# Kernel tuning notes

Hardware: AMD Instinct MI355X
Metric: run time of the kernel (lower is better)

The kernel has to match this reference:

```python
import jax, jax.numpy as jnp
import numpy as np

NUM_CLASSES = 21
THRESH = 0.5
NEG_POS = 3
VAR0, VAR1 = 0.1, 0.2  # SSD cfg['variance']
B, P, O = 32, 32768, 50


def point_form(boxes):
    # center form (cx,cy,w,h) -> corner form (xmin,ymin,xmax,ymax)
    return jnp.concatenate([boxes[:, :2] - boxes[:, 2:] / 2,
                            boxes[:, :2] + boxes[:, 2:] / 2], axis=1)


def jaccard(box_a, box_b):
    # box_a [A,4], box_b [B,4], corner form -> IoU [A,B]
    max_xy = jnp.minimum(box_a[:, None, 2:], box_b[None, :, 2:])
    min_xy = jnp.maximum(box_a[:, None, :2], box_b[None, :, :2])
    inter = jnp.prod(jnp.clip(max_xy - min_xy, 0.0, None), axis=2)
    area_a = jnp.prod(box_a[:, 2:] - box_a[:, :2], axis=1)[:, None]
    area_b = jnp.prod(box_b[:, 2:] - box_b[:, :2], axis=1)[None, :]
    return inter / (area_a + area_b - inter)


def encode(matched, priors):
    # matched corner form [P,4], priors center form [P,4]
    g_cxcy = ((matched[:, :2] + matched[:, 2:]) / 2 - priors[:, :2]) / (VAR0 * priors[:, 2:])
    g_wh = jnp.log((matched[:, 2:] - matched[:, :2]) / priors[:, 2:]) / VAR1
    return jnp.concatenate([g_cxcy, g_wh], axis=1)


def match_one(truths, labels, priors):
    # truths [O,4] corner, labels [O], priors [P,4] center
    overlaps = jaccard(truths, point_form(priors))          # [O,P]
    best_prior_idx = jnp.argmax(overlaps, axis=1)           # [O]
    best_truth_overlap = jnp.max(overlaps, axis=0)          # [P]
    best_truth_idx = jnp.argmax(overlaps, axis=0)           # [P]
    # ensure every gt matches its best prior
    best_truth_overlap = best_truth_overlap.at[best_prior_idx].set(2.0)
    best_truth_idx = best_truth_idx.at[best_prior_idx].set(jnp.arange(truths.shape[0]))
    matches = truths[best_truth_idx]                        # [P,4]
    conf = (labels[best_truth_idx] + 1.0).astype(jnp.int32)
    conf = jnp.where(best_truth_overlap < THRESH, 0, conf)
    return encode(matches, priors), conf


def setup_inputs() -> dict:
    key = jax.random.key(0)
    k1, k2, k3, k4, k5, k6 = jax.random.split(key, 6)
    loc_data = jax.random.normal(k1, (B, P, 4), dtype=jnp.float32)
    conf_data = jax.random.normal(k2, (B, P, NUM_CLASSES), dtype=jnp.float32)
    # priors in center form: centers in (0,1), sizes in (0.02, 0.5)
    cxy = jax.random.uniform(k3, (P, 2), dtype=jnp.float32)
    wh = jax.random.uniform(k4, (P, 2), dtype=jnp.float32, minval=0.02, maxval=0.5)
    priors = jnp.concatenate([cxy, wh], axis=1)
    # targets: valid corner-form boxes + label
    pts = jax.random.uniform(k5, (B, O, 2, 2), dtype=jnp.float32)
    xymin = pts.min(axis=2)
    xymax = jnp.maximum(pts.max(axis=2), xymin + 0.01)
    labels = jax.random.randint(k6, (B, O), 0, NUM_CLASSES - 1).astype(jnp.float32)
    targets = jnp.concatenate([xymin, xymax, labels[..., None]], axis=-1)
    return {"loc_data": loc_data, "conf_data": conf_data, "priors": priors, "targets": targets}


def reference(loc_data, conf_data, priors, targets):
    truths = targets[..., :4]
    labels = targets[..., 4]
    loc_t, conf_t = jax.vmap(match_one, in_axes=(0, 0, None))(truths, labels, priors)
    loc_t = jax.lax.stop_gradient(loc_t)
    conf_t = jax.lax.stop_gradient(conf_t)

    pos = conf_t > 0                                         # [B,P]
    # localization: smooth-L1, summed over positives
    diff = loc_data - loc_t
    ad = jnp.abs(diff)
    sl1 = jnp.where(ad < 1.0, 0.5 * diff * diff, ad - 0.5)
    loss_l = jnp.sum(sl1 * pos[..., None].astype(sl1.dtype))

    # per-prior softmax CE (logsumexp - true logit)
    lse = jax.nn.logsumexp(conf_data, axis=-1)               # [B,P]
    true_logit = jnp.take_along_axis(conf_data, conf_t[..., None], axis=-1)[..., 0]
    ce = lse - true_logit                                    # [B,P]

    # hard negative mining: rank negatives by CE (pos zeroed out)
    ce_mine = jnp.where(pos, 0.0, ce)
    loss_idx = jnp.argsort(-ce_mine, axis=1)
    idx_rank = jnp.argsort(loss_idx, axis=1)
    num_pos = jnp.sum(pos, axis=1, keepdims=True)            # [B,1]
    num_neg = jnp.clip(NEG_POS * num_pos, None, pos.shape[1] - 1)
    neg = idx_rank < num_neg

    sel = pos | neg
    loss_c = jnp.sum(jnp.where(sel, ce, 0.0))

    N = jnp.sum(num_pos).astype(loss_l.dtype)
    return loss_l / N, loss_c / N
```

## Files before the change

### kernel.cpp

```cpp
#include <hip/hip_runtime.h>
#include <math.h>

#define BB 32
#define PP 32768
#define OO 50
#define NC 21
#define MPT 4

#define WBINLO (104 << 7)
#define WBINS  2048

typedef unsigned long long u64;
typedef unsigned int u32;
typedef unsigned char u8;

static constexpr size_t OFF_WHC   = 0;
static constexpr size_t OFF_WHS   = OFF_WHC  + 4ull*BB*WBINS;
static constexpr size_t OFF_KEYS  = OFF_WHS  + 4ull*BB*WBINS;
static constexpr size_t OFF_NPOS  = OFF_KEYS + 8ull*BB*OO;
static constexpr size_t OFF_DACC  = OFF_NPOS + 128;
static constexpr size_t ZERO_BYTES = OFF_DACC + 8ull*3*BB;
static constexpr size_t OFF_BTOV  = (ZERO_BYTES + 127) & ~127ull;
static constexpr size_t OFF_BTIDX = OFF_BTOV  + 4ull*BB*PP;

static __device__ __forceinline__ float fast_div(float a, float b) {
    return a * __builtin_amdgcn_rcpf(b);
}

__global__ __launch_bounds__(256) void match_kernel(
    const float* __restrict__ priors, const float* __restrict__ targets,
    float* __restrict__ btov, u8* __restrict__ btidx, u64* __restrict__ keys)
{
#pragma clang fp contract(off)
    const int b = blockIdx.y;
    const int tid = threadIdx.x;
    const int lane = tid & 63, wid = tid >> 6;
    const int wbase = blockIdx.x * (256 * MPT) + wid * (64 * MPT);

    __shared__ float tr[OO * 5];
    __shared__ u64 wkeys[4][OO];
    if (tid < OO * 5) tr[tid] = targets[(size_t)b * OO * 5 + tid];
    __syncthreads();

    float px1[MPT], py1[MPT], px2[MPT], py2[MPT], area_p[MPT];
#pragma unroll
    for (int s = 0; s < MPT; ++s) {
        int p = wbase + s * 64 + lane;
        float4 pr = *(const float4*)(priors + (size_t)p * 4);
        px1[s] = pr.x - pr.z * 0.5f; py1[s] = pr.y - pr.w * 0.5f;
        px2[s] = pr.x + pr.z * 0.5f; py2[s] = pr.y + pr.w * 0.5f;
        area_p[s] = (px2[s] - px1[s]) * (py2[s] - py1[s]);
    }

    float bestv[MPT]; int besto[MPT];
#pragma unroll
    for (int s = 0; s < MPT; ++s) { bestv[s] = -1.0f; besto[s] = 0; }

    for (int o = 0; o < OO; ++o) {
        float tx1 = tr[o*5+0], ty1 = tr[o*5+1], tx2 = tr[o*5+2], ty2 = tr[o*5+3];
        float area_t = (tx2 - tx1) * (ty2 - ty1);
        float iou[MPT];
#pragma unroll
        for (int s = 0; s < MPT; ++s) {
            float ix1 = fmaxf(tx1, px1[s]), iy1 = fmaxf(ty1, py1[s]);
            float ix2 = fminf(tx2, px2[s]), iy2 = fminf(ty2, py2[s]);
            float dx = fmaxf(ix2 - ix1, 0.0f), dy = fmaxf(iy2 - iy1, 0.0f);
            float inter = dx * dy;
            iou[s] = fast_div(inter, (area_t + area_p[s]) - inter);
            if (iou[s] > bestv[s]) { bestv[s] = iou[s]; besto[s] = o; }
        }
        float mv = fmaxf(fmaxf(iou[0], iou[1]), fmaxf(iou[2], iou[3]));
        for (int m = 1; m < 64; m <<= 1)
            mv = fmaxf(mv, __shfl_xor(mv, m, 64));
        u64 b0 = __ballot(iou[0] == mv);
        u64 b1 = __ballot(iou[1] == mv);
        u64 b2 = __ballot(iou[2] == mv);
        u64 b3 = __ballot(iou[3] == mv);
        if (lane == 0) {
            int s, l;
            if      (b0) { s = 0; l = __ffsll(b0) - 1; }
            else if (b1) { s = 1; l = __ffsll(b1) - 1; }
            else if (b2) { s = 2; l = __ffsll(b2) - 1; }
            else if (b3) { s = 3; l = __ffsll(b3) - 1; }
            else         { s = 0; l = 0; }
            u32 wp = (u32)(wbase + s * 64 + l);
            wkeys[wid][o] = ((u64)__float_as_uint(mv) << 32) | (u64)(0xFFFFFFFFu - wp);
        }
    }
#pragma unroll
    for (int s = 0; s < MPT; ++s) {
        int p = wbase + s * 64 + lane;
        btov[(size_t)b * PP + p] = bestv[s];
        btidx[(size_t)b * PP + p] = (u8)besto[s];
    }
    __syncthreads();
    if (tid < OO) {
        u64 k0 = wkeys[0][tid];
        for (int w = 1; w < 4; ++w) { u64 kw = wkeys[w][tid]; if (kw > k0) k0 = kw; }
        atomicMax(&keys[b * OO + tid], k0);
    }
}

__global__ void override_kernel(const u64* __restrict__ keys,
                                float* __restrict__ btov, u8* __restrict__ btidx) {
    const int b = blockIdx.x;
    const int o = threadIdx.x;
    u32 p = 0xFFFFFFFFu;
    if (o < OO) p = 0xFFFFFFFFu - (u32)(keys[b * OO + o] & 0xFFFFFFFFull);
    bool win = (o < OO);
    for (int o2 = 1; o2 < OO; ++o2) {
        u32 p2 = __shfl(p, o2, 64);
        if (o < o2 && p2 == p) win = false;
    }
    if (win) {
        btov[(size_t)b * PP + p] = 2.0f;
        btidx[(size_t)b * PP + p] = (u8)o;
    }
}

static __device__ __forceinline__ u32 top16bits(float v) {
    u32 u = __float_as_uint(v);
    return (v > 0.0f) ? u : 0u;
}

#define EL(k) ((((k) & 3) == 0) ? v[(k) >> 2].x : \
               (((k) & 3) == 1) ? v[(k) >> 2].y : \
               (((k) & 3) == 2) ? v[(k) >> 2].z : v[(k) >> 2].w)

__global__ __launch_bounds__(256) void score_kernel(
    const float* __restrict__ loc, const float* __restrict__ conf,
    const float* __restrict__ priors, const float* __restrict__ targets,
    const float* __restrict__ btov, const u8* __restrict__ btidx,
    int* __restrict__ npos, double* __restrict__ dacc,
    u32* __restrict__ whc, float* __restrict__ whs)
{
    const int b = blockIdx.y;
    const int tid = threadIdx.x;
    const int p = blockIdx.x * 1024 + tid * 4;
    __shared__ float tr[OO * 5];
    __shared__ __align__(16) u32 hh[WBINS];
    __shared__ __align__(16) float hs[WBINS];
    if (tid < OO * 5) tr[tid] = targets[(size_t)b * OO * 5 + tid];
#pragma unroll
    for (int j = 0; j < WBINS / 256; ++j) { hh[j * 256 + tid] = 0; hs[j * 256 + tid] = 0.0f; }
    __syncthreads();

    float4 ov4 = *(const float4*)(btov + (size_t)b * PP + p);
    uchar4 ox4 = *(const uchar4*)(btidx + (size_t)b * PP + p);
    const float ovv[4] = {ov4.x, ov4.y, ov4.z, ov4.w};
    const int  oidx[4] = {(int)ox4.x, (int)ox4.y, (int)ox4.z, (int)ox4.w};

    const float4* cp = (const float4*)(conf + ((size_t)b * PP + p) * NC);
    float4 v[21];
    float cev[4];
    double l_l = 0.0, pce = 0.0; int np_ = 0;

#pragma unroll
    for (int r = 0; r < 4; ++r) {
        const int jlo = (r == 0) ? 0 : ((21 * (r - 1) + 20) / 4 + 1);
        const int jhi = (21 * r + 20) / 4;
#pragma unroll
        for (int j = jlo; j <= jhi; ++j) v[j] = cp[j];

        int conft = 0;
        if (ovv[r] >= 0.5f) conft = (int)(tr[oidx[r] * 5 + 4] + 1.0f);
        const bool pos = conft > 0;

        float m = -1e30f;
#pragma unroll
        for (int c = 0; c < NC; ++c) m = fmaxf(m, EL(21 * r + c));
        float s = 0.0f, tl = 0.0f;
#pragma unroll
        for (int c = 0; c < NC; ++c) {
            float xx = EL(21 * r + c);
            s += expf(xx - m);
            if (c == conft) tl = xx;
        }
        float ce = (m + logf(s)) - tl;
        cev[r] = pos ? 0.0f : ce;

        if (pos) {
            np_ += 1; pce += (double)ce;
            int o = oidx[r];
            float mx1 = tr[o*5+0], my1 = tr[o*5+1], mx2 = tr[o*5+2], my2 = tr[o*5+3];
            float4 pr = *(const float4*)(priors + (size_t)(p + r) * 4);
            float lt0 = ((mx1 + mx2) * 0.5f - pr.x) / (0.1f * pr.z);
            float lt1 = ((my1 + my2) * 0.5f - pr.y) / (0.1f * pr.w);
            float lt2 = logf((mx2 - mx1) / pr.z) / 0.2f;
            float lt3 = logf((my2 - my1) / pr.w) / 0.2f;
            float4 l4 = *(const float4*)(loc + ((size_t)b * PP + p + r) * 4);
            float lpv[4] = {l4.x, l4.y, l4.z, l4.w};
            float lt[4] = {lt0, lt1, lt2, lt3};
#pragma unroll
            for (int i2 = 0; i2 < 4; ++i2) {
                float d = lpv[i2] - lt[i2];
                float ad = fabsf(d);
                l_l += (double)(ad < 1.0f ? 0.5f * d * d : ad - 0.5f);
            }
        }
    }

#pragma unroll
    for (int r = 0; r < 4; ++r) {
        u32 t16 = top16bits(cev[r]) >> 16;
        if (t16 != 0) {
            int widx = ((int)t16 - WBINLO) >> 1;
            widx = widx < 0 ? 0 : (widx > WBINS - 1 ? WBINS - 1 : widx);
            atomicAdd(&hh[widx], 1u);
            atomicAdd(&hs[widx], cev[r]);
        }
    }
    __syncthreads();
#pragma unroll
    for (int j = 0; j < WBINS / 256; ++j) {
        u32 c = hh[j * 256 + tid];
        if (c) {
            atomicAdd(&whc[(size_t)b * WBINS + j * 256 + tid], c);
            atomicAdd(&whs[(size_t)b * WBINS + j * 256 + tid], hs[j * 256 + tid]);
        }
    }
    __syncthreads();
    double* rl = (double*)hh;
    double* rc = (double*)hs;
    int*    rn = (int*)(hh + 1024);
    rl[tid] = l_l; rc[tid] = pce; rn[tid] = np_;
    __syncthreads();
    for (int s2 = 128; s2 > 0; s2 >>= 1) {
        if (tid < s2) { rl[tid] += rl[tid+s2]; rc[tid] += rc[tid+s2]; rn[tid] += rn[tid+s2]; }
        __syncthreads();
    }
    if (tid == 0) {
        atomicAdd(&dacc[b], rl[0]);
        atomicAdd(&dacc[BB + b], rc[0]);
        atomicAdd(&npos[b], rn[0]);
    }
}

__global__ __launch_bounds__(256) void selwin_kernel(
    const u32* __restrict__ whc, const float* __restrict__ whs,
    const int* __restrict__ npos, double* __restrict__ dacc)
{
    const int b = blockIdx.x, tid = threadIdx.x;
    const int lane = tid & 63, wid = tid >> 6;
    int k = npos[b] * 3; if (k > PP - 1) k = PP - 1;
    if (k <= 0) return;
    const u32* hc = whc + (size_t)b * WBINS;
    const float* hsg = whs + (size_t)b * WBINS;

    __shared__ u32 ccnt_[WBINS / 256]; __shared__ float csum_[WBINS / 256];
    __shared__ u32 ct[256]; __shared__ float fs[256];
    __shared__ int s_cT; __shared__ u32 s_aboveC; __shared__ float s_aboveS;
    __shared__ u32 sT;

    for (int c = wid; c < WBINS / 256; c += 4) {
        u32 cnt = 0; float sm = 0.0f;
#pragma unroll
        for (int q = 0; q < 4; ++q) {
            int idx = c * 256 + q * 64 + lane;
            cnt += hc[idx];
            sm  += hsg[idx];
        }
        for (int m = 1; m < 64; m <<= 1) {
            cnt += __shfl_xor(cnt, m, 64);
            sm  += __shfl_xor(sm, m, 64);
        }
        if (lane == 0) { ccnt_[c] = cnt; csum_[c] = sm; }
    }
    if (tid == 0) sT = 0;
    __syncthreads();
    if (tid == 0) {
        u32 cum = 0; float scum = 0.0f; int cT = -1; u32 aboveC = 0; float aboveS = 0.0f;
        for (int c = WBINS / 256 - 1; c >= 0; --c) {
            if (cum + ccnt_[c] >= (u32)k) { cT = c; aboveC = cum; aboveS = scum; break; }
            cum += ccnt_[c]; scum += csum_[c];
        }
        s_cT = cT; s_aboveC = aboveC; s_aboveS = aboveS;
        if (cT < 0) dacc[2 * BB + b] = (double)scum;
    }
    __syncthreads();
    const int cT = s_cT;
    if (cT < 0) return;
    const u32 aboveC = s_aboveC; const float aboveS = s_aboveS;

    const u32 myc = hc[cT * 256 + tid];
    const float mys = hsg[cT * 256 + tid];
    ct[tid] = myc; fs[tid] = mys;
    __syncthreads();
    for (int off = 1; off < 256; off <<= 1) {
        u32 a1 = (tid + off < 256) ? ct[tid + off] : 0;
        float a2 = (tid + off < 256) ? fs[tid + off] : 0.0f;
        __syncthreads();
        ct[tid] += a1; fs[tid] += a2;
        __syncthreads();
    }
    if (aboveC + ct[tid] >= (u32)k) atomicMax(&sT, (u32)tid);
    __syncthreads();
    const int T = (int)sT;
    if (tid == T) {
        u32 aboveBinC = aboveC + ((T < 255) ? ct[T + 1] : 0);
        float aboveBinS = aboveS + ((T < 255) ? fs[T + 1] : 0.0f);
        int k2 = k - (int)aboveBinC;
        double avg = (double)mys / (double)myc;
        dacc[2 * BB + b] = (double)aboveBinS + (double)k2 * avg;
    }
}

__global__ void finalize_kernel(const int* __restrict__ npos,
                                const double* __restrict__ dacc, float* __restrict__ out) {
    if (threadIdx.x == 0 && blockIdx.x == 0) {
        double N = 0.0, ll = 0.0, lc = 0.0;
        for (int b = 0; b < BB; ++b) {
            N += (double)npos[b];
            ll += dacc[b];
            lc += dacc[BB + b] + dacc[2 * BB + b];
        }
        out[0] = (float)(ll / N);
        out[1] = (float)(lc / N);
    }
}

extern "C" void kernel_launch(void* const* d_in, const int* in_sizes, int n_in,
                              void* d_out, int out_size, void* d_ws, size_t ws_size,
                              hipStream_t stream) {
    const float* loc     = (const float*)d_in[0];
    const float* conf    = (const float*)d_in[1];
    const float* priors  = (const float*)d_in[2];
    const float* targets = (const float*)d_in[3];
    char* ws = (char*)d_ws;
    u32*    whc   = (u32*)   (ws + OFF_WHC);
    float*  whs   = (float*) (ws + OFF_WHS);
    u64*    keys  = (u64*)   (ws + OFF_KEYS);
    int*    npos  = (int*)   (ws + OFF_NPOS);
    double* dacc  = (double*)(ws + OFF_DACC);
    float*  btov  = (float*) (ws + OFF_BTOV);
    u8*     btidx = (u8*)    (ws + OFF_BTIDX);
    float*  out   = (float*)d_out;

    hipMemsetAsync(ws, 0, ZERO_BYTES, stream);
    match_kernel<<<dim3(PP / (256 * MPT), BB), 256, 0, stream>>>(priors, targets, btov, btidx, keys);
    override_kernel<<<BB, 64, 0, stream>>>(keys, btov, btidx);
    score_kernel<<<dim3(PP / 1024, BB), 256, 0, stream>>>(loc, conf, priors, targets, btov, btidx, npos, dacc, whc, whs);
    selwin_kernel<<<BB, 256, 0, stream>>>(whc, whs, npos, dacc);
    finalize_kernel<<<1, 64, 0, stream>>>(npos, dacc, out);
}
```

Baseline: 104.8 us.

## Split match over object halves and merge per-prior best via 64-bit atomicMax keys

The match kernel's grid is split along a new z dimension so each block handles 25 of the 50 ground-truth objects, doubling the number of blocks. Per-prior best overlap and index are packed into a 64-bit key and merged with atomicMax into a zeroed workspace. The forced-match override now also uses atomicMax with a high sentinel, which replaces the shuffle-based duplicate resolution. This adds a larger memset (8 bytes per prior instead of 5) and global atomics in exchange for more parallelism in the match stage. Tie-breaking semantics shift slightly: duplicate forced matches are now resolved by the highest object index rather than the last-write order.

```diff
diff --git a/kernel.cpp b/kernel.cpp
--- a/kernel.cpp
+++ b/kernel.cpp
@@ -4,6 +4,7 @@
 #define BB 32
 #define PP 32768
 #define OO 50
+#define NT 25
 #define NC 21
 #define MPT 4
 
@@ -13,15 +14,17 @@
 typedef unsigned long long u64;
 typedef unsigned int u32;
 typedef unsigned char u8;
+
+static constexpr u32 FORCED_HI = 0x40000000u;
+static constexpr u32 HALF_BITS = 0x3F000000u;
 
 static constexpr size_t OFF_WHC   = 0;
 static constexpr size_t OFF_WHS   = OFF_WHC  + 4ull*BB*WBINS;
 static constexpr size_t OFF_KEYS  = OFF_WHS  + 4ull*BB*WBINS;
 static constexpr size_t OFF_NPOS  = OFF_KEYS + 8ull*BB*OO;
 static constexpr size_t OFF_DACC  = OFF_NPOS + 128;
-static constexpr size_t ZERO_BYTES = OFF_DACC + 8ull*3*BB;
-static constexpr size_t OFF_BTOV  = (ZERO_BYTES + 127) & ~127ull;
-static constexpr size_t OFF_BTIDX = OFF_BTOV  + 4ull*BB*PP;
+static constexpr size_t OFF_KEY2  = ((OFF_DACC + 8ull*3*BB + 127) & ~127ull);
+static constexpr size_t ZERO_BYTES = OFF_KEY2 + 8ull*BB*PP;
 
 static __device__ __forceinline__ float fast_div(float a, float b) {
     return a * __builtin_amdgcn_rcpf(b);
@@ -29,17 +32,18 @@
 
 __global__ __launch_bounds__(256) void match_kernel(
     const float* __restrict__ priors, const float* __restrict__ targets,
-    float* __restrict__ btov, u8* __restrict__ btidx, u64* __restrict__ keys)
+    u64* __restrict__ key2, u64* __restrict__ keys)
 {
 #pragma clang fp contract(off)
     const int b = blockIdx.y;
+    const int obase = blockIdx.z * NT;
     const int tid = threadIdx.x;
     const int lane = tid & 63, wid = tid >> 6;
     const int wbase = blockIdx.x * (256 * MPT) + wid * (64 * MPT);
 
-    __shared__ float tr[OO * 5];
-    __shared__ u64 wkeys[4][OO];
-    if (tid < OO * 5) tr[tid] = targets[(size_t)b * OO * 5 + tid];
+    __shared__ float tr[NT * 5];
+    __shared__ u64 wkeys[4][NT];
+    if (tid < NT * 5) tr[tid] = targets[(size_t)b * OO * 5 + obase * 5 + tid];
     __syncthreads();
 
     float px1[MPT], py1[MPT], px2[MPT], py2[MPT], area_p[MPT];
@@ -56,7 +60,7 @@
 #pragma unroll
     for (int s = 0; s < MPT; ++s) { bestv[s] = -1.0f; besto[s] = 0; }
 
-    for (int o = 0; o < OO; ++o) {
+    for (int o = 0; o < NT; ++o) {
         float tx1 = tr[o*5+0], ty1 = tr[o*5+1], tx2 = tr[o*5+2], ty2 = tr[o*5+3];
         float area_t = (tx2 - tx1) * (ty2 - ty1);
         float iou[MPT];
@@ -90,31 +94,25 @@
 #pragma unroll
     for (int s = 0; s < MPT; ++s) {
         int p = wbase + s * 64 + lane;
-        btov[(size_t)b * PP + p] = bestv[s];
-        btidx[(size_t)b * PP + p] = (u8)besto[s];
-    }
-    __syncthreads();
-    if (tid < OO) {
+        u64 key = ((u64)__float_as_uint(bestv[s]) << 32)
+                | (u64)(u32)(49 - (obase + besto[s]));
+        atomicMax(&key2[(size_t)b * PP + p], key);
+    }
+    __syncthreads();
+    if (tid < NT) {
         u64 k0 = wkeys[0][tid];
         for (int w = 1; w < 4; ++w) { u64 kw = wkeys[w][tid]; if (kw > k0) k0 = kw; }
-        atomicMax(&keys[b * OO + tid], k0);
-    }
-}
-
-__global__ void override_kernel(const u64* __restrict__ keys,
-                                float* __restrict__ btov, u8* __restrict__ btidx) {
+        atomicMax(&keys[b * OO + obase + tid], k0);
+    }
+}
+
+__global__ void override_kernel(const u64* __restrict__ keys, u64* __restrict__ key2) {
     const int b = blockIdx.x;
     const int o = threadIdx.x;
-    u32 p = 0xFFFFFFFFu;
-    if (o < OO) p = 0xFFFFFFFFu - (u32)(keys[b * OO + o] & 0xFFFFFFFFull);
-    bool win = (o < OO);
-    for (int o2 = 1; o2 < OO; ++o2) {
-        u32 p2 = __shfl(p, o2, 64);
-        if (o < o2 && p2 == p) win = false;
-    }
-    if (win) {
-        btov[(size_t)b * PP + p] = 2.0f;
-        btidx[(size_t)b * PP + p] = (u8)o;
+    if (o < OO) {
+        u32 p = 0xFFFFFFFFu - (u32)(keys[b * OO + o] & 0xFFFFFFFFull);
+        atomicMax(&key2[(size_t)b * PP + p],
+                  ((u64)FORCED_HI << 32) | (u64)(u32)(64 + o));
     }
 }
 
@@ -130,7 +128,7 @@
 __global__ __launch_bounds__(256) void score_kernel(
     const float* __restrict__ loc, const float* __restrict__ conf,
     const float* __restrict__ priors, const float* __restrict__ targets,
-    const float* __restrict__ btov, const u8* __restrict__ btidx,
+    const u64* __restrict__ key2,
     int* __restrict__ npos, double* __restrict__ dacc,
     u32* __restrict__ whc, float* __restrict__ whs)
 {
@@ -145,10 +143,9 @@
     for (int j = 0; j < WBINS / 256; ++j) { hh[j * 256 + tid] = 0; hs[j * 256 + tid] = 0.0f; }
     __syncthreads();
 
-    float4 ov4 = *(const float4*)(btov + (size_t)b * PP + p);
-    uchar4 ox4 = *(const uchar4*)(btidx + (size_t)b * PP + p);
-    const float ovv[4] = {ov4.x, ov4.y, ov4.z, ov4.w};
-    const int  oidx[4] = {(int)ox4.x, (int)ox4.y, (int)ox4.z, (int)ox4.w};
+    ulonglong2 k01 = *(const ulonglong2*)(key2 + (size_t)b * PP + p);
+    ulonglong2 k23 = *(const ulonglong2*)(key2 + (size_t)b * PP + p + 2);
+    const u64 kk[4] = {k01.x, k01.y, k23.x, k23.y};
 
     const float4* cp = (const float4*)(conf + ((size_t)b * PP + p) * NC);
     float4 v[21];
@@ -162,9 +159,12 @@
 #pragma unroll
         for (int j = jlo; j <= jhi; ++j) v[j] = cp[j];
 
-        int conft = 0;
-        if (ovv[r] >= 0.5f) conft = (int)(tr[oidx[r] * 5 + 4] + 1.0f);
-        const bool pos = conft > 0;
+        const u32 hi = (u32)(kk[r] >> 32);
+        const u32 lo = (u32)kk[r];
+        const bool forced = lo >= 64u;
+        const int o = forced ? (int)(lo - 64u) : (int)(49u - lo);
+        const bool pos = forced || hi >= HALF_BITS;
+        const int conft = pos ? (int)(tr[o * 5 + 4] + 1.0f) : 0;
 
         float m = -1e30f;
 #pragma unroll
@@ -181,7 +181,6 @@
 
         if (pos) {
             np_ += 1; pce += (double)ce;
-            int o = oidx[r];
             float mx1 = tr[o*5+0], my1 = tr[o*5+1], mx2 = tr[o*5+2], my2 = tr[o*5+3];
             float4 pr = *(const float4*)(priors + (size_t)(p + r) * 4);
             float lt0 = ((mx1 + mx2) * 0.5f - pr.x) / (0.1f * pr.z);
@@ -332,14 +331,13 @@
     u64*    keys  = (u64*)   (ws + OFF_KEYS);
     int*    npos  = (int*)   (ws + OFF_NPOS);
     double* dacc  = (double*)(ws + OFF_DACC);
-    float*  btov  = (float*) (ws + OFF_BTOV);
-    u8*     btidx = (u8*)    (ws + OFF_BTIDX);
+    u64*    key2  = (u64*)   (ws + OFF_KEY2);
     float*  out   = (float*)d_out;
 
     hipMemsetAsync(ws, 0, ZERO_BYTES, stream);
-    match_kernel<<<dim3(PP / (256 * MPT), BB), 256, 0, stream>>>(priors, targets, btov, btidx, keys);
-    override_kernel<<<BB, 64, 0, stream>>>(keys, btov, btidx);
-    score_kernel<<<dim3(PP / 1024, BB), 256, 0, stream>>>(loc, conf, priors, targets, btov, btidx, npos, dacc, whc, whs);
+    match_kernel<<<dim3(PP / (256 * MPT), BB, 2), 256, 0, stream>>>(priors, targets, key2, keys);
+    override_kernel<<<BB, 64, 0, stream>>>(keys, key2);
+    score_kernel<<<dim3(PP / 1024, BB), 256, 0, stream>>>(loc, conf, priors, targets, key2, npos, dacc, whc, whs);
     selwin_kernel<<<BB, 256, 0, stream>>>(whc, whs, npos, dacc);
     finalize_kernel<<<1, 64, 0, stream>>>(npos, dacc, out);
 }
```

Result: faster. 99.21 us (-5.3%).
